# Performance work log

Hardware: AMD Instinct MI355X
Metric: run time of the kernel (lower is better)

Reference implementation:

```python
import jax, jax.numpy as jnp
import numpy as np

B, N, D, H, FF = 4, 1024, 512, 8, 2048
DH = D // H
RPE_HID = 16
COORD_DIM = 2


def _ln(x, g, b, eps=1e-5):
    m = jnp.mean(x, axis=-1, keepdims=True)
    v = jnp.mean((x - m) ** 2, axis=-1, keepdims=True)
    return (x - m) * jax.lax.rsqrt(v + eps) * g + b


def setup_inputs() -> dict:
    key = jax.random.key(0)
    ks = jax.random.split(key, 20)
    s = 0.02
    inp = {
        "x": jax.random.normal(ks[0], (B, N, D), dtype=jnp.float32),
        "coords": jax.random.uniform(ks[1], (B, N, COORD_DIM), dtype=jnp.float32),
        # qkv + output projections
        "Wq": jax.random.normal(ks[2], (D, D), jnp.float32) * s,
        "bq": jnp.zeros((D,), jnp.float32),
        "Wk": jax.random.normal(ks[3], (D, D), jnp.float32) * s,
        "bk": jnp.zeros((D,), jnp.float32),
        "Wv": jax.random.normal(ks[4], (D, D), jnp.float32) * s,
        "bv": jnp.zeros((D,), jnp.float32),
        "Wo": jax.random.normal(ks[5], (D, D), jnp.float32) * s,
        "bo": jnp.zeros((D,), jnp.float32),
        # learned per-head logit scale (Swin-v2 style cosine attention)
        "logit_scale": jnp.full((H, 1, 1), np.log(10.0), jnp.float32),
        # absolute positional embedder PE: Linear(2 -> D)
        "W_pe": jax.random.normal(ks[6], (COORD_DIM, D), jnp.float32) * s,
        "b_pe": jnp.zeros((D,), jnp.float32),
        # relative positional embedder RPE: MLP(2 -> 16 -> H)
        "W_r1": jax.random.normal(ks[7], (COORD_DIM, RPE_HID), jnp.float32) * 0.5,
        "b_r1": jnp.zeros((RPE_HID,), jnp.float32),
        "W_r2": jax.random.normal(ks[8], (RPE_HID, H), jnp.float32) * 0.5,
        "b_r2": jnp.zeros((H,), jnp.float32),
        # layernorm params
        "g_peq": jnp.ones((D,), jnp.float32), "bt_peq": jnp.zeros((D,), jnp.float32),
        "g_pek": jnp.ones((D,), jnp.float32), "bt_pek": jnp.zeros((D,), jnp.float32),
        "g2": jnp.ones((D,), jnp.float32), "bt2": jnp.zeros((D,), jnp.float32),
        "g3": jnp.ones((D,), jnp.float32), "bt3": jnp.zeros((D,), jnp.float32),
        # MLP (bias=False)
        "W_ff1": jax.random.normal(ks[9], (D, FF), jnp.float32) * s,
        "W_ff2": jax.random.normal(ks[10], (FF, D), jnp.float32) * s,
    }
    return inp


def reference(x, coords, Wq, bq, Wk, bk, Wv, bv, Wo, bo, logit_scale,
              W_pe, b_pe, W_r1, b_r1, W_r2, b_r2,
              g_peq, bt_peq, g_pek, bt_pek, g2, bt2, g3, bt3,
              W_ff1, W_ff2):
    # --- PE add + LayerNorm on q and k (self-attention: coords_cross_ = coords)
    pe = coords @ W_pe + b_pe                      # [B,N,D]
    q = _ln(x + pe, g_peq, bt_peq)
    k = _ln(x + pe, g_pek, bt_pek)
    v = x                                          # v is NOT PE-normed in source

    # --- relative-position bias from cartesian coord differences
    rel = coords[:, :, None, :] - coords[:, None, :, :]   # [B,Nq,Nk,2]
    hid = jax.nn.relu(rel @ W_r1 + b_r1)                  # [B,Nq,Nk,16]
    bias = hid @ W_r2 + b_r2                              # [B,Nq,Nk,H]
    bias = jnp.transpose(bias, (0, 3, 1, 2))              # [B,H,Nq,Nk]

    # --- multi-head cosine attention with learned logit scale
    qp = (q @ Wq + bq).reshape(B, N, H, DH)
    kp = (k @ Wk + bk).reshape(B, N, H, DH)
    vp = (v @ Wv + bv).reshape(B, N, H, DH)
    qn = qp / jnp.maximum(jnp.linalg.norm(qp, axis=-1, keepdims=True), 1e-12)
    kn = kp / jnp.maximum(jnp.linalg.norm(kp, axis=-1, keepdims=True), 1e-12)
    scale = jnp.exp(jnp.minimum(logit_scale, jnp.log(100.0)))  # [H,1,1]
    attn = jnp.einsum('bqhd,bkhd->bhqk', qn, kn) * scale[None] + bias
    attn = jax.nn.softmax(attn, axis=-1)
    att_out = jnp.einsum('bhqk,bkhd->bqhd', attn, vp).reshape(B, N, D)
    att_out = att_out @ Wo + bo

    # --- residual + norm + MLP (LeakyReLU 0.2 after each linear) + residual + norm
    x1 = _ln(x + att_out, g2, bt2)
    mlp = jax.nn.leaky_relu(
        jax.nn.leaky_relu(x1 @ W_ff1, 0.2) @ W_ff2, 0.2)
    return _ln(x1 + mlp, g3, bt3)
```

## Files before the change

kernel.cpp:

```cpp
#include <hip/hip_runtime.h>

#define BB 4
#define NN 1024
#define DD 512
#define HH 8
#define DHH 64
#define FFF 2048

typedef __attribute__((ext_vector_type(8))) short bf16x8;
typedef __attribute__((ext_vector_type(4))) float f32x4;

__device__ inline float wave_sum(float v) {
#pragma unroll
  for (int off = 32; off; off >>= 1) v += __shfl_xor(v, off);
  return v;
}

__device__ inline unsigned short cvt_bf16(float f) {
  union { float f; unsigned u; } x;
  x.f = f;
  unsigned r = x.u + 0x7FFFu + ((x.u >> 16) & 1u);
  return (unsigned short)(r >> 16);
}

__device__ __forceinline__ void gl_lds16(const void* g, void* l) {
  __builtin_amdgcn_global_load_lds(
      (__attribute__((address_space(1))) void*)(g),
      (__attribute__((address_space(3))) void*)(l), 16, 0, 0);
}

__global__ __launch_bounds__(256) void wconv_kernel(
    const float* __restrict__ W0, const float* __restrict__ W1,
    const float* __restrict__ W2, const float* __restrict__ W3,
    const float* __restrict__ W4, const float* __restrict__ W5,
    unsigned short* __restrict__ out) {
  int bidx = blockIdx.x;
  const float* W; unsigned short* Wt; int K, N, local;
  if (bidx < 256) {
    int sel = bidx >> 6; local = bidx & 63;
    W = sel == 0 ? W0 : sel == 1 ? W1 : sel == 2 ? W2 : W3;
    K = 512; N = 512; Wt = out + (size_t)sel * 262144;
  } else if (bidx < 512) {
    local = bidx - 256; W = W4; K = 512; N = 2048; Wt = out + 1048576;
  } else {
    local = bidx - 512; W = W5; K = 2048; N = 512; Wt = out + 2097152;
  }
  int ntn = N >> 6;
  int tn = (local & (ntn - 1)) << 6, tk = (local / ntn) << 6;
  __shared__ float tile[64][65];
  int tid = threadIdx.x;
#pragma unroll
  for (int i = 0; i < 16; ++i) {
    int e = tid + i * 256, kk = e >> 6, nn = e & 63;
    tile[kk][nn] = W[(size_t)(tk + kk) * N + tn + nn];
  }
  __syncthreads();
#pragma unroll
  for (int i = 0; i < 16; ++i) {
    int e = tid + i * 256, nn = e >> 6, kk = e & 63;
    Wt[(size_t)(tn + nn) * K + tk + kk] = cvt_bf16(tile[kk][nn]);
  }
}

__global__ __launch_bounds__(256) void bias_kernel(
    const float* __restrict__ coords,
    const float* __restrict__ W_r1, const float* __restrict__ b_r1,
    const float* __restrict__ W_r2, const float* __restrict__ b_r2,
    unsigned short* __restrict__ bias_out) {
  int kt = blockIdx.x, qt = blockIdx.y, b = blockIdx.z;
  int tid = threadIdx.x;
  int q = qt * 64 + (tid >> 2);
  int k0 = kt * 32 + (tid & 3) * 8;
  float cq0 = coords[((size_t)b * NN + q) * 2 + 0];
  float cq1 = coords[((size_t)b * NN + q) * 2 + 1];
  float Aq[16];
#pragma unroll
  for (int l = 0; l < 16; ++l)
    Aq[l] = fmaf(cq0, W_r1[l], fmaf(cq1, W_r1[16 + l], b_r1[l]));
  float ck0[8], ck1[8];
#pragma unroll
  for (int kk = 0; kk < 8; ++kk) {
    ck0[kk] = coords[((size_t)b * NN + k0 + kk) * 2 + 0];
    ck1[kk] = coords[((size_t)b * NN + k0 + kk) * 2 + 1];
  }
  float acc[8][8];
#pragma unroll
  for (int kk = 0; kk < 8; ++kk)
#pragma unroll
    for (int h = 0; h < 8; ++h) acc[kk][h] = b_r2[h];
#pragma unroll
  for (int l = 0; l < 16; ++l) {
    float w1a = W_r1[l], w1b = W_r1[16 + l];
#pragma unroll
    for (int kk = 0; kk < 8; ++kk) {
      float hv = Aq[l] - fmaf(ck0[kk], w1a, ck1[kk] * w1b);
      hv = fmaxf(hv, 0.f);
#pragma unroll
      for (int h = 0; h < 8; ++h)
        acc[kk][h] = fmaf(hv, W_r2[l * HH + h], acc[kk][h]);
    }
  }
#pragma unroll
  for (int h = 0; h < 8; ++h) {
    bf16x8 ov;
#pragma unroll
    for (int kk = 0; kk < 8; ++kk) ov[kk] = (short)cvt_bf16(acc[kk][h]);
    *(bf16x8*)&bias_out[(((size_t)b * HH + h) * NN + q) * NN + k0] = ov;
  }
}

__global__ __launch_bounds__(512) void pe_ln_kernel(
    const float* __restrict__ x, const float* __restrict__ coords,
    const float* __restrict__ W_pe, const float* __restrict__ b_pe,
    const float* __restrict__ g_q, const float* __restrict__ bt_q,
    const float* __restrict__ g_k, const float* __restrict__ bt_k,
    unsigned short* __restrict__ q_lnb, unsigned short* __restrict__ k_lnb,
    unsigned short* __restrict__ x_bf) {
  int row = blockIdx.x;
  int tid = threadIdx.x;
  float c0 = coords[(size_t)row * 2 + 0];
  float c1 = coords[(size_t)row * 2 + 1];
  size_t idx = (size_t)row * DD + tid;
  float xv = x[idx];
  x_bf[idx] = cvt_bf16(xv);
  float val = xv + c0 * W_pe[tid] + c1 * W_pe[DD + tid] + b_pe[tid];

  __shared__ float ws[8], ws2[8];
  float s = wave_sum(val);
  if ((tid & 63) == 0) ws[tid >> 6] = s;
  __syncthreads();
  float mean = 0.f;
#pragma unroll
  for (int w = 0; w < 8; ++w) mean += ws[w];
  mean *= (1.f / DD);
  float dv = val - mean;
  float s2 = wave_sum(dv * dv);
  if ((tid & 63) == 0) ws2[tid >> 6] = s2;
  __syncthreads();
  float var = 0.f;
#pragma unroll
  for (int w = 0; w < 8; ++w) var += ws2[w];
  var *= (1.f / DD);
  float rstd = rsqrtf(var + 1e-5f);
  q_lnb[idx] = cvt_bf16(dv * rstd * g_q[tid] + bt_q[tid]);
  k_lnb[idx] = cvt_bf16(dv * rstd * g_k[tid] + bt_k[tid]);
}

__global__ __launch_bounds__(512) void add_ln_kernel(
    const float* __restrict__ a, const float* __restrict__ r,
    const float* __restrict__ g, const float* __restrict__ bt,
    float* __restrict__ out, unsigned short* __restrict__ out_bf) {
  int row = blockIdx.x;
  int tid = threadIdx.x;
  size_t idx = (size_t)row * DD + tid;
  float val = a[idx] + r[idx];
  __shared__ float ws[8], ws2[8];
  float s = wave_sum(val);
  if ((tid & 63) == 0) ws[tid >> 6] = s;
  __syncthreads();
  float mean = 0.f;
#pragma unroll
  for (int w = 0; w < 8; ++w) mean += ws[w];
  mean *= (1.f / DD);
  float dv = val - mean;
  float s2 = wave_sum(dv * dv);
  if ((tid & 63) == 0) ws2[tid >> 6] = s2;
  __syncthreads();
  float var = 0.f;
#pragma unroll
  for (int w = 0; w < 8; ++w) var += ws2[w];
  var *= (1.f / DD);
  float rstd = rsqrtf(var + 1e-5f);
  float o = dv * rstd * g[tid] + bt[tid];
  out[idx] = o;
  if (out_bf) out_bf[idx] = cvt_bf16(o);
}

template <int ACT, int EPI>
__global__ __launch_bounds__(256) void mgemm_kernel(
    const unsigned short* __restrict__ A, const unsigned short* __restrict__ BT,
    const float* __restrict__ bias, void* __restrict__ C,
    int M, int Nc, int K) {
  __shared__ unsigned short lds[4][8192];
  int tid = threadIdx.x;
  int w = tid >> 6, lane = tid & 63, lg = lane >> 4, lr = lane & 15;
  int bm = blockIdx.y * 128, bn = blockIdx.x * 128;
  int wr = w >> 1, wc = w & 1;

  int segl = lane >> 3;
  int cb = (lane & 7) << 4;

  f32x4 zf = {0.f, 0.f, 0.f, 0.f};
  f32x4 acc[4][4];
#pragma unroll
  for (int mi = 0; mi < 4; ++mi)
#pragma unroll
    for (int ni = 0; ni < 4; ++ni) acc[mi][ni] = zf;

  int nt = K >> 6;

  auto STAGE = [&](int buf, int t) {
    int k0 = t << 6;
#pragma unroll
    for (int i = 0; i < 4; ++i) {
      int seg = w * 4 + i;
      int r = (seg << 3) + segl;
      int csw = cb ^ ((r & 7) << 4);
      const char* ga = (const char*)A + (((size_t)(bm + r) * K + k0) << 1) + csw;
      gl_lds16(ga, &lds[buf * 2][seg << 9]);
      const char* gb = (const char*)BT + (((size_t)(bn + r) * K + k0) << 1) + csw;
      gl_lds16(gb, &lds[buf * 2 + 1][seg << 9]);
    }
  };

  auto COMPUTE = [&](int buf) {
    const unsigned short* As = lds[buf * 2];
    const unsigned short* Bs = lds[buf * 2 + 1];
    bf16x8 af[2][4], bfr[2][4];
#pragma unroll
    for (int kh = 0; kh < 2; ++kh)
#pragma unroll
      for (int mi = 0; mi < 4; ++mi) {
        int r = wr * 64 + mi * 16 + lr;
        int e = (r << 6) + (kh << 5) + (lg << 3);
        af[kh][mi] = *(const bf16x8*)&As[e ^ ((r & 7) << 3)];
        int rb = wc * 64 + mi * 16 + lr;
        int eb = (rb << 6) + (kh << 5) + (lg << 3);
        bfr[kh][mi] = *(const bf16x8*)&Bs[eb ^ ((rb & 7) << 3)];
      }
#pragma unroll
    for (int kh = 0; kh < 2; ++kh)
#pragma unroll
      for (int mi = 0; mi < 4; ++mi)
#pragma unroll
        for (int ni = 0; ni < 4; ++ni)
          acc[mi][ni] = __builtin_amdgcn_mfma_f32_16x16x32_bf16(
              af[kh][mi], bfr[kh][ni], acc[mi][ni], 0, 0, 0);
  };

  STAGE(0, 0);
  __syncthreads();
  for (int t = 0; t < nt; ++t) {
    if (t + 1 < nt) STAGE((t + 1) & 1, t + 1);
    COMPUTE(t & 1);
    __syncthreads();
  }

#pragma unroll
  for (int ni = 0; ni < 4; ++ni) {
    int col = bn + wc * 64 + ni * 16 + lr;
    float bv = bias ? bias[col] : 0.f;
#pragma unroll
    for (int mi = 0; mi < 4; ++mi) {
#pragma unroll
      for (int j = 0; j < 4; ++j) {
        int row = bm + wr * 64 + mi * 16 + lg * 4 + j;
        float v = acc[mi][ni][j] + bv;
        if (ACT == 1) v = v > 0.f ? v : 0.2f * v;
        if (EPI == 1)
          ((unsigned short*)C)[(size_t)row * Nc + col] = cvt_bf16(v);
        else
          ((float*)C)[(size_t)row * Nc + col] = v;
      }
    }
  }
}

__global__ __launch_bounds__(256) void qkv_gemm_kernel(
    const unsigned short* __restrict__ q_lnb,
    const unsigned short* __restrict__ k_lnb,
    const unsigned short* __restrict__ x_bf,
    const unsigned short* __restrict__ wt,
    const float* __restrict__ bq, const float* __restrict__ bk,
    const float* __restrict__ bv_,
    unsigned short* __restrict__ q_bf, unsigned short* __restrict__ k_bf,
    unsigned short* __restrict__ vt_g) {
  int z = blockIdx.z;
  const unsigned short* A = z == 0 ? q_lnb : z == 1 ? k_lnb : x_bf;
  const unsigned short* BT = wt + (size_t)z * 262144;
  const float* bias = z == 0 ? bq : z == 1 ? bk : bv_;

  __shared__ unsigned short lds[4][8192];
  int tid = threadIdx.x;
  int w = tid >> 6, lane = tid & 63, lg = lane >> 4, lr = lane & 15;
  int bm = blockIdx.y * 128, bn = blockIdx.x * 128;
  int wr = w >> 1, wc = w & 1;
  int segl = lane >> 3;
  int cb = (lane & 7) << 4;

  f32x4 zf = {0.f, 0.f, 0.f, 0.f};
  f32x4 acc[4][4];
#pragma unroll
  for (int mi = 0; mi < 4; ++mi)
#pragma unroll
    for (int ni = 0; ni < 4; ++ni) acc[mi][ni] = zf;

  auto STAGE = [&](int buf, int t) {
    int k0 = t << 6;
#pragma unroll
    for (int i = 0; i < 4; ++i) {
      int seg = w * 4 + i;
      int r = (seg << 3) + segl;
      int csw = cb ^ ((r & 7) << 4);
      const char* ga = (const char*)A + (((size_t)(bm + r) * DD + k0) << 1) + csw;
      gl_lds16(ga, &lds[buf * 2][seg << 9]);
      const char* gb = (const char*)BT + (((size_t)(bn + r) * DD + k0) << 1) + csw;
      gl_lds16(gb, &lds[buf * 2 + 1][seg << 9]);
    }
  };
  auto COMPUTE = [&](int buf) {
    const unsigned short* As = lds[buf * 2];
    const unsigned short* Bs = lds[buf * 2 + 1];
    bf16x8 af[2][4], bfr[2][4];
#pragma unroll
    for (int kh = 0; kh < 2; ++kh)
#pragma unroll
      for (int mi = 0; mi < 4; ++mi) {
        int r = wr * 64 + mi * 16 + lr;
        int e = (r << 6) + (kh << 5) + (lg << 3);
        af[kh][mi] = *(const bf16x8*)&As[e ^ ((r & 7) << 3)];
        int rb = wc * 64 + mi * 16 + lr;
        int eb = (rb << 6) + (kh << 5) + (lg << 3);
        bfr[kh][mi] = *(const bf16x8*)&Bs[eb ^ ((rb & 7) << 3)];
      }
#pragma unroll
    for (int kh = 0; kh < 2; ++kh)
#pragma unroll
      for (int mi = 0; mi < 4; ++mi)
#pragma unroll
        for (int ni = 0; ni < 4; ++ni)
          acc[mi][ni] = __builtin_amdgcn_mfma_f32_16x16x32_bf16(
              af[kh][mi], bfr[kh][ni], acc[mi][ni], 0, 0, 0);
  };

  STAGE(0, 0);
  __syncthreads();
  for (int t = 0; t < 8; ++t) {
    if (t + 1 < 8) STAGE((t + 1) & 1, t + 1);
    COMPUTE(t & 1);
    __syncthreads();
  }

  int h = (bn >> 6) + wc;
  float bvf[4];
#pragma unroll
  for (int ni = 0; ni < 4; ++ni) bvf[ni] = bias[bn + wc * 64 + ni * 16 + lr];
#pragma unroll
  for (int mi = 0; mi < 4; ++mi) {
#pragma unroll
    for (int j = 0; j < 4; ++j) {
      float vals[4]; float ss = 0.f;
#pragma unroll
      for (int ni = 0; ni < 4; ++ni) {
        float v = acc[mi][ni][j] + bvf[ni];
        vals[ni] = v;
        ss = fmaf(v, v, ss);
      }
      int row = bm + wr * 64 + mi * 16 + lg * 4 + j;
      int b_ = row >> 10, n_ = row & (NN - 1);
      if (z <= 1) {
        ss += __shfl_xor(ss, 1);
        ss += __shfl_xor(ss, 2);
        ss += __shfl_xor(ss, 4);
        ss += __shfl_xor(ss, 8);
        float rn = 1.f / fmaxf(sqrtf(ss), 1e-12f);
        unsigned short* ob = (z == 0 ? q_bf : k_bf) +
                             (((size_t)b_ * HH + h) * NN + n_) * DHH;
#pragma unroll
        for (int ni = 0; ni < 4; ++ni)
          ob[ni * 16 + lr] = cvt_bf16(vals[ni] * rn);
      } else {
#pragma unroll
        for (int ni = 0; ni < 4; ++ni)
          vt_g[(((size_t)b_ * HH + h) * DHH + ni * 16 + lr) * NN + n_] =
              cvt_bf16(vals[ni]);
      }
    }
  }
}

template <int NSPLIT>
__global__ __launch_bounds__(256) void attn_wave_kernel(
    const unsigned short* __restrict__ qb, const unsigned short* __restrict__ kb,
    const unsigned short* __restrict__ vtg,
    const unsigned short* __restrict__ bias_g,
    const float* __restrict__ logit_scale,
    unsigned short* __restrict__ attb,
    unsigned short* __restrict__ part, int nb) {
  int qt = blockIdx.x, h = blockIdx.y;
  int b = blockIdx.z % nb, sp = blockIdx.z / nb;
  int tid = threadIdx.x;
  int w = tid >> 6, lane = tid & 63;
  int lg = lane >> 4, lr = lane & 15;

  __shared__ unsigned short pl[4][1024];

  const size_t bh = ((size_t)b * HH + h) * NN;
  const size_t vbase = ((size_t)b * HH + h) * DHH * NN;
  const int NT = (NN / 64) / NSPLIT;
  const int kt0 = sp * NT;

  int q_glob = qt * 64 + w * 16 + lr;
  bf16x8 aq0 = *(const bf16x8*)&qb[(bh + q_glob) * DHH + lg * 8];
  bf16x8 aq1 = *(const bf16x8*)&qb[(bh + q_glob) * DHH + 32 + lg * 8];

  float scale_h = __expf(fminf(logit_scale[h], 4.605170185988091f));

  const unsigned short* brow[4];
#pragma unroll
  for (int r = 0; r < 4; ++r)
    brow[r] = &bias_g[(bh + qt * 64 + w * 16 + lg * 4 + r) * NN + lr];

  float m_run[4] = {-1e30f, -1e30f, -1e30f, -1e30f};
  float l_run[4] = {0.f, 0.f, 0.f, 0.f};
  f32x4 zf = {0.f, 0.f, 0.f, 0.f};
  f32x4 acc_o[4] = {zf, zf, zf, zf};

  unsigned short bu[4][4];
#pragma unroll
  for (int r = 0; r < 4; ++r)
#pragma unroll
    for (int kc = 0; kc < 4; ++kc) bu[kc][r] = brow[r][kt0 * 64 + kc * 16];

#pragma unroll 2
  for (int t = 0; t < NT; ++t) {
    int ktg = kt0 + t;

    f32x4 s_acc[4];
#pragma unroll
    for (int kc = 0; kc < 4; ++kc) {
      const unsigned short* krow =
          &kb[(bh + ktg * 64 + kc * 16 + lr) * DHH + lg * 8];
      bf16x8 bk0 = *(const bf16x8*)krow;
      bf16x8 bk1 = *(const bf16x8*)(krow + 32);
      s_acc[kc] = __builtin_amdgcn_mfma_f32_16x16x32_bf16(aq0, bk0, zf, 0, 0, 0);
      s_acc[kc] = __builtin_amdgcn_mfma_f32_16x16x32_bf16(aq1, bk1, s_acc[kc], 0, 0, 0);
    }

    unsigned short bu2[4][4];
    if (t + 1 < NT) {
#pragma unroll
      for (int r = 0; r < 4; ++r)
#pragma unroll
        for (int kc = 0; kc < 4; ++kc)
          bu2[kc][r] = brow[r][(ktg + 1) * 64 + kc * 16];
    }

#pragma unroll
    for (int kc = 0; kc < 4; ++kc)
#pragma unroll
      for (int r = 0; r < 4; ++r) {
        float bf_ = __uint_as_float(((unsigned)bu[kc][r]) << 16);
        s_acc[kc][r] = fmaf(s_acc[kc][r], scale_h, bf_);
      }

    float pf[4][4];
#pragma unroll
    for (int r = 0; r < 4; ++r) {
      float mx = fmaxf(fmaxf(s_acc[0][r], s_acc[1][r]),
                       fmaxf(s_acc[2][r], s_acc[3][r]));
      mx = fmaxf(mx, __shfl_xor(mx, 1));
      mx = fmaxf(mx, __shfl_xor(mx, 2));
      mx = fmaxf(mx, __shfl_xor(mx, 4));
      mx = fmaxf(mx, __shfl_xor(mx, 8));
      float m_new = fmaxf(m_run[r], mx);
      float alpha = __expf(m_run[r] - m_new);
      m_run[r] = m_new;
      float ps = 0.f;
#pragma unroll
      for (int kc = 0; kc < 4; ++kc) {
        float p = __expf(s_acc[kc][r] - m_new);
        pf[kc][r] = p;
        ps += p;
      }
      l_run[r] = l_run[r] * alpha + ps;
#pragma unroll
      for (int ds = 0; ds < 4; ++ds) acc_o[ds][r] *= alpha;
    }

#pragma unroll
    for (int kc = 0; kc < 4; ++kc)
#pragma unroll
      for (int r = 0; r < 4; ++r) {
        int q = lg * 4 + r;
        pl[w][(q * 64 + kc * 16 + lr) ^ ((q & 7) << 3)] = cvt_bf16(pf[kc][r]);
      }

#pragma unroll
    for (int ka = 0; ka < 2; ++ka) {
      bf16x8 pa = *(const bf16x8*)&pl[w][(lr * 64 + ka * 32 + lg * 8) ^
                                         ((lr & 7) << 3)];
#pragma unroll
      for (int ds = 0; ds < 4; ++ds) {
        int d = ds * 16 + lr;
        bf16x8 bv = *(const bf16x8*)&vtg[vbase + (size_t)d * NN +
                                         ktg * 64 + ka * 32 + lg * 8];
        acc_o[ds] = __builtin_amdgcn_mfma_f32_16x16x32_bf16(pa, bv, acc_o[ds], 0, 0, 0);
      }
    }

    if (t + 1 < NT) {
#pragma unroll
      for (int r = 0; r < 4; ++r)
#pragma unroll
        for (int kc = 0; kc < 4; ++kc) bu[kc][r] = bu2[kc][r];
    }
  }

#pragma unroll
  for (int r = 0; r < 4; ++r) {
    l_run[r] += __shfl_xor(l_run[r], 1);
    l_run[r] += __shfl_xor(l_run[r], 2);
    l_run[r] += __shfl_xor(l_run[r], 4);
    l_run[r] += __shfl_xor(l_run[r], 8);
  }

  if (NSPLIT == 1) {
#pragma unroll
    for (int ds = 0; ds < 4; ++ds)
#pragma unroll
      for (int r = 0; r < 4; ++r) {
        int qg = qt * 64 + w * 16 + lg * 4 + r;
        attb[((size_t)b * NN + qg) * DD + h * DHH + ds * 16 + lr] =
            cvt_bf16(acc_o[ds][r] / l_run[r]);
      }
  } else {
#pragma unroll
    for (int r = 0; r < 4; ++r) {
      int qg = qt * 64 + w * 16 + lg * 4 + r;
      size_t idx = ((size_t)(sp * nb + b) * HH + h) * NN + qg;
      unsigned short* pr = part + idx * 68;
#pragma unroll
      for (int ds = 0; ds < 4; ++ds)
        pr[ds * 16 + lr] = cvt_bf16(acc_o[ds][r]);
      if (lr == 0) {
        *(float*)(pr + 64) = m_run[r];
        *(float*)(pr + 66) = l_run[r];
      }
    }
  }
}

__global__ __launch_bounds__(256) void combine_kernel(
    const unsigned short* __restrict__ part, unsigned short* __restrict__ attb,
    int nb) {
  int tid = threadIdx.x;
  int w = tid >> 6, d = tid & 63;
  int row = blockIdx.x * 4 + w;
  int b = row >> 13, rem = row & 8191, h = rem >> 10, n = rem & (NN - 1);
  size_t i0 = ((size_t)b * HH + h) * NN + n;
  size_t i1 = i0 + (size_t)nb * HH * NN;
  const unsigned short* p0 = part + i0 * 68;
  const unsigned short* p1 = part + i1 * 68;
  float m0 = *(const float*)(p0 + 64), l0 = *(const float*)(p0 + 66);
  float m1 = *(const float*)(p1 + 64), l1 = *(const float*)(p1 + 66);
  float ms = fmaxf(m0, m1);
  float w0 = __expf(m0 - ms), w1 = __expf(m1 - ms);
  float a0 = __uint_as_float(((unsigned)p0[d]) << 16);
  float a1 = __uint_as_float(((unsigned)p1[d]) << 16);
  float o = (a0 * w0 + a1 * w1) / (l0 * w0 + l1 * w1);
  attb[((size_t)b * NN + n) * DD + h * DHH + d] = cvt_bf16(o);
}

extern "C" void kernel_launch(void* const* d_in, const int* in_sizes, int n_in,
                              void* d_out, int out_size, void* d_ws, size_t ws_size,
                              hipStream_t stream) {
  const float* x      = (const float*)d_in[0];
  const float* coords = (const float*)d_in[1];
  const float* Wq = (const float*)d_in[2];  const float* bq = (const float*)d_in[3];
  const float* Wk = (const float*)d_in[4];  const float* bk = (const float*)d_in[5];
  const float* Wv = (const float*)d_in[6];  const float* bv = (const float*)d_in[7];
  const float* Wo = (const float*)d_in[8];  const float* bo = (const float*)d_in[9];
  const float* logit_scale = (const float*)d_in[10];
  const float* W_pe = (const float*)d_in[11]; const float* b_pe = (const float*)d_in[12];
  const float* W_r1 = (const float*)d_in[13]; const float* b_r1 = (const float*)d_in[14];
  const float* W_r2 = (const float*)d_in[15]; const float* b_r2 = (const float*)d_in[16];
  const float* g_peq = (const float*)d_in[17]; const float* bt_peq = (const float*)d_in[18];
  const float* g_pek = (const float*)d_in[19]; const float* bt_pek = (const float*)d_in[20];
  const float* g2 = (const float*)d_in[21]; const float* bt2 = (const float*)d_in[22];
  const float* g3 = (const float*)d_in[23]; const float* bt3 = (const float*)d_in[24];
  const float* W_ff1 = (const float*)d_in[25];
  const float* W_ff2 = (const float*)d_in[26];
  float* out = (float*)d_out;

  const size_t T = (size_t)BB * NN;
  char* wsb = (char*)d_ws;
  const size_t U = 4u * 1024u * 1024u;

  unsigned short* wt_all = (unsigned short*)(wsb + 0 * U);
  unsigned short* WoT   = wt_all + 786432;
  unsigned short* Wff1T = wt_all + 1048576;
  unsigned short* Wff2T = wt_all + 2097152;
  unsigned short* q_lnb = (unsigned short*)(wsb + 2 * U);
  unsigned short* k_lnb = (unsigned short*)(wsb + 3 * U);
  unsigned short* x_bf  = (unsigned short*)(wsb + 4 * U);
  unsigned short* q_bf  = (unsigned short*)(wsb + 5 * U);
  unsigned short* k_bf  = (unsigned short*)(wsb + 6 * U);
  unsigned short* v_bf  = (unsigned short*)(wsb + 7 * U);
  unsigned short* att_bf = (unsigned short*)(wsb + 8 * U);
  float* proj = (float*)(wsb + 9 * U);
  float* x1   = (float*)(wsb + 11 * U);
  unsigned short* x1_bf = (unsigned short*)(wsb + 13 * U);
  unsigned short* hid_bf = (unsigned short*)(wsb + 2 * U);
  float* mlp  = (float*)(wsb + 9 * U);
  unsigned short* part_ws = (unsigned short*)(wsb + 2 * U);
  unsigned short* bias_ws = (unsigned short*)(wsb + 9 * U);

  const int full_path = (ws_size >= 25 * U) ? 1 : 0;

  wconv_kernel<<<dim3(768), dim3(256), 0, stream>>>(
      Wq, Wk, Wv, Wo, W_ff1, W_ff2, wt_all);

  pe_ln_kernel<<<dim3(T), dim3(512), 0, stream>>>(
      x, coords, W_pe, b_pe, g_peq, bt_peq, g_pek, bt_pek, q_lnb, k_lnb, x_bf);

  qkv_gemm_kernel<<<dim3(DD / 128, T / 128, 3), dim3(256), 0, stream>>>(
      q_lnb, k_lnb, x_bf, wt_all, bq, bk, bv, q_bf, k_bf, v_bf);

  if (full_path) {
    bias_kernel<<<dim3(NN / 32, NN / 64, BB), dim3(256), 0, stream>>>(
        coords, W_r1, b_r1, W_r2, b_r2, bias_ws);
    attn_wave_kernel<2><<<dim3(NN / 64, HH, 2 * BB), dim3(256), 0, stream>>>(
        q_bf, k_bf, v_bf, bias_ws, logit_scale, nullptr, part_ws, BB);
    combine_kernel<<<dim3(BB * HH * NN / 4), dim3(256), 0, stream>>>(
        part_ws, att_bf, BB);
  } else {
    for (int b = 0; b < BB; ++b) {
      bias_kernel<<<dim3(NN / 32, NN / 64, 1), dim3(256), 0, stream>>>(
          coords + (size_t)b * NN * 2, W_r1, b_r1, W_r2, b_r2, bias_ws);
      attn_wave_kernel<1><<<dim3(NN / 64, HH, 1), dim3(256), 0, stream>>>(
          q_bf + (size_t)b * HH * NN * DHH, k_bf + (size_t)b * HH * NN * DHH,
          v_bf + (size_t)b * HH * DHH * NN, bias_ws, logit_scale,
          att_bf + (size_t)b * NN * DD, nullptr, 1);
    }
  }

  mgemm_kernel<0, 0><<<dim3(DD / 128, T / 128), dim3(256), 0, stream>>>(
      att_bf, WoT, bo, proj, (int)T, DD, DD);

  add_ln_kernel<<<dim3(T), dim3(512), 0, stream>>>(x, proj, g2, bt2, x1, x1_bf);

  mgemm_kernel<1, 1><<<dim3(FFF / 128, T / 128), dim3(256), 0, stream>>>(
      x1_bf, Wff1T, nullptr, hid_bf, (int)T, FFF, DD);
  mgemm_kernel<1, 0><<<dim3(DD / 128, T / 128), dim3(256), 0, stream>>>(
      hid_bf, Wff2T, nullptr, mlp, (int)T, DD, FFF);

  add_ln_kernel<<<dim3(T), dim3(512), 0, stream>>>(x1, mlp, g3, bt3, out, nullptr);
}
```

Measured before the change: 198.1 us.

## Store RPE bias in 64x64 tiles and stage it through LDS

The bias kernel now writes the relative-position bias in contiguous 64x64 tiles per (batch, head, q-tile, k-tile) instead of row-major [Nq,Nk]. The attention kernel loads each tile with coalesced 16-byte vector loads and writes it into a double-buffered, XOR-swizzled per-wave LDS buffer, then reads scalar values from LDS. The goal is to replace the 16 strided 2-byte global loads per lane per tile with wide coalesced loads. In exchange it uses more LDS and drops the unroll-by-2 pragma.

```diff
diff --git a/kernel.cpp b/kernel.cpp
--- a/kernel.cpp
+++ b/kernel.cpp
@@ -69,7 +69,8 @@
     unsigned short* __restrict__ bias_out) {
   int kt = blockIdx.x, qt = blockIdx.y, b = blockIdx.z;
   int tid = threadIdx.x;
-  int q = qt * 64 + (tid >> 2);
+  int qL = tid >> 2;
+  int q = qt * 64 + qL;
   int k0 = kt * 32 + (tid & 3) * 8;
   float cq0 = coords[((size_t)b * NN + q) * 2 + 0];
   float cq1 = coords[((size_t)b * NN + q) * 2 + 1];
@@ -100,12 +101,14 @@
         acc[kk][h] = fmaf(hv, W_r2[l * HH + h], acc[kk][h]);
     }
   }
+  int elem = qL * 64 + (kt & 1) * 32 + (tid & 3) * 8;
 #pragma unroll
   for (int h = 0; h < 8; ++h) {
     bf16x8 ov;
 #pragma unroll
     for (int kk = 0; kk < 8; ++kk) ov[kk] = (short)cvt_bf16(acc[kk][h]);
-    *(bf16x8*)&bias_out[(((size_t)b * HH + h) * NN + q) * NN + k0] = ov;
+    size_t tile = (((size_t)b * HH + h) * 16 + qt) * 16 + (kt >> 1);
+    *(bf16x8*)&bias_out[tile * 4096 + elem] = ov;
   }
 }
 
@@ -383,7 +386,7 @@
 __global__ __launch_bounds__(256) void attn_wave_kernel(
     const unsigned short* __restrict__ qb, const unsigned short* __restrict__ kb,
     const unsigned short* __restrict__ vtg,
-    const unsigned short* __restrict__ bias_g,
+    const unsigned short* __restrict__ bias_t,
     const float* __restrict__ logit_scale,
     unsigned short* __restrict__ attb,
     unsigned short* __restrict__ part, int nb) {
@@ -393,38 +396,49 @@
   int w = tid >> 6, lane = tid & 63;
   int lg = lane >> 4, lr = lane & 15;
 
+  __shared__ unsigned short bl[4][2][1024];
   __shared__ unsigned short pl[4][1024];
 
   const size_t bh = ((size_t)b * HH + h) * NN;
   const size_t vbase = ((size_t)b * HH + h) * DHH * NN;
   const int NT = (NN / 64) / NSPLIT;
   const int kt0 = sp * NT;
+  const unsigned short* bsrc0 =
+      bias_t + ((((size_t)b * HH + h) * 16 + qt) * 16 + kt0) * 4096 +
+      w * 1024 + lane * 8;
+
+  int rr0 = lane >> 3, rr1 = 8 + (lane >> 3);
+  int d0 = (rr0 * 8 + ((lane & 7) ^ (rr0 & 7))) * 8;
+  int d1 = (rr1 * 8 + ((lane & 7) ^ (rr1 & 7))) * 8;
 
   int q_glob = qt * 64 + w * 16 + lr;
   bf16x8 aq0 = *(const bf16x8*)&qb[(bh + q_glob) * DHH + lg * 8];
   bf16x8 aq1 = *(const bf16x8*)&qb[(bh + q_glob) * DHH + 32 + lg * 8];
 
   float scale_h = __expf(fminf(logit_scale[h], 4.605170185988091f));
-
-  const unsigned short* brow[4];
-#pragma unroll
-  for (int r = 0; r < 4; ++r)
-    brow[r] = &bias_g[(bh + qt * 64 + w * 16 + lg * 4 + r) * NN + lr];
 
   float m_run[4] = {-1e30f, -1e30f, -1e30f, -1e30f};
   float l_run[4] = {0.f, 0.f, 0.f, 0.f};
   f32x4 zf = {0.f, 0.f, 0.f, 0.f};
   f32x4 acc_o[4] = {zf, zf, zf, zf};
 
-  unsigned short bu[4][4];
-#pragma unroll
-  for (int r = 0; r < 4; ++r)
-#pragma unroll
-    for (int kc = 0; kc < 4; ++kc) bu[kc][r] = brow[r][kt0 * 64 + kc * 16];
-
-#pragma unroll 2
+  {
+    bf16x8 br0 = *(const bf16x8*)bsrc0;
+    bf16x8 br1 = *(const bf16x8*)(bsrc0 + 512);
+    *(bf16x8*)&bl[w][0][d0] = br0;
+    *(bf16x8*)&bl[w][0][d1] = br1;
+  }
+
   for (int t = 0; t < NT; ++t) {
+    int cur = t & 1;
     int ktg = kt0 + t;
+
+    bf16x8 nb0, nb1;
+    if (t + 1 < NT) {
+      const unsigned short* bs = bsrc0 + (size_t)(t + 1) * 4096;
+      nb0 = *(const bf16x8*)bs;
+      nb1 = *(const bf16x8*)(bs + 512);
+    }
 
     f32x4 s_acc[4];
 #pragma unroll
@@ -437,20 +451,14 @@
       s_acc[kc] = __builtin_amdgcn_mfma_f32_16x16x32_bf16(aq1, bk1, s_acc[kc], 0, 0, 0);
     }
 
-    unsigned short bu2[4][4];
-    if (t + 1 < NT) {
-#pragma unroll
-      for (int r = 0; r < 4; ++r)
-#pragma unroll
-        for (int kc = 0; kc < 4; ++kc)
-          bu2[kc][r] = brow[r][(ktg + 1) * 64 + kc * 16];
-    }
-
 #pragma unroll
     for (int kc = 0; kc < 4; ++kc)
 #pragma unroll
       for (int r = 0; r < 4; ++r) {
-        float bf_ = __uint_as_float(((unsigned)bu[kc][r]) << 16);
+        int rr = lg * 4 + r;
+        unsigned short ub =
+            bl[w][cur][(rr * 64 + kc * 16 + lr) ^ ((rr & 7) << 3)];
+        float bf_ = __uint_as_float(((unsigned)ub) << 16);
         s_acc[kc][r] = fmaf(s_acc[kc][r], scale_h, bf_);
       }
 
@@ -500,10 +508,8 @@
     }
 
     if (t + 1 < NT) {
-#pragma unroll
-      for (int r = 0; r < 4; ++r)
-#pragma unroll
-        for (int kc = 0; kc < 4; ++kc) bu[kc][r] = bu2[kc][r];
+      *(bf16x8*)&bl[w][cur ^ 1][d0] = nb0;
+      *(bf16x8*)&bl[w][cur ^ 1][d1] = nb1;
     }
   }
 
```

After: 195.4 us. About the same (-1.4%).

## Fuse relative-position bias MLP into attention kernel instead of materializing bias

Applied to the files above, without the earlier changes.

Removes the separate bias kernel, which wrote a bf16 [B,H,N,N] bias tensor that attention then read back. The per-position first-layer terms (Aq with bias, Ck) are now precomputed in the LN kernel, and attention recomputes the 16-hidden ReLU MLP inline per score for its own head. This cuts a large HBM write and read at the cost of roughly 16 extra FMA/max ops per score per head, which repeats the hidden-layer work across the 8 heads. The workspace-size fallback path is dropped and the split-2 path always runs.

```diff
diff --git a/kernel.cpp b/kernel.cpp
--- a/kernel.cpp
+++ b/kernel.cpp
@@ -62,64 +62,25 @@
   }
 }
 
-__global__ __launch_bounds__(256) void bias_kernel(
-    const float* __restrict__ coords,
-    const float* __restrict__ W_r1, const float* __restrict__ b_r1,
-    const float* __restrict__ W_r2, const float* __restrict__ b_r2,
-    unsigned short* __restrict__ bias_out) {
-  int kt = blockIdx.x, qt = blockIdx.y, b = blockIdx.z;
-  int tid = threadIdx.x;
-  int q = qt * 64 + (tid >> 2);
-  int k0 = kt * 32 + (tid & 3) * 8;
-  float cq0 = coords[((size_t)b * NN + q) * 2 + 0];
-  float cq1 = coords[((size_t)b * NN + q) * 2 + 1];
-  float Aq[16];
-#pragma unroll
-  for (int l = 0; l < 16; ++l)
-    Aq[l] = fmaf(cq0, W_r1[l], fmaf(cq1, W_r1[16 + l], b_r1[l]));
-  float ck0[8], ck1[8];
-#pragma unroll
-  for (int kk = 0; kk < 8; ++kk) {
-    ck0[kk] = coords[((size_t)b * NN + k0 + kk) * 2 + 0];
-    ck1[kk] = coords[((size_t)b * NN + k0 + kk) * 2 + 1];
-  }
-  float acc[8][8];
-#pragma unroll
-  for (int kk = 0; kk < 8; ++kk)
-#pragma unroll
-    for (int h = 0; h < 8; ++h) acc[kk][h] = b_r2[h];
-#pragma unroll
-  for (int l = 0; l < 16; ++l) {
-    float w1a = W_r1[l], w1b = W_r1[16 + l];
-#pragma unroll
-    for (int kk = 0; kk < 8; ++kk) {
-      float hv = Aq[l] - fmaf(ck0[kk], w1a, ck1[kk] * w1b);
-      hv = fmaxf(hv, 0.f);
-#pragma unroll
-      for (int h = 0; h < 8; ++h)
-        acc[kk][h] = fmaf(hv, W_r2[l * HH + h], acc[kk][h]);
-    }
-  }
-#pragma unroll
-  for (int h = 0; h < 8; ++h) {
-    bf16x8 ov;
-#pragma unroll
-    for (int kk = 0; kk < 8; ++kk) ov[kk] = (short)cvt_bf16(acc[kk][h]);
-    *(bf16x8*)&bias_out[(((size_t)b * HH + h) * NN + q) * NN + k0] = ov;
-  }
-}
-
 __global__ __launch_bounds__(512) void pe_ln_kernel(
     const float* __restrict__ x, const float* __restrict__ coords,
     const float* __restrict__ W_pe, const float* __restrict__ b_pe,
+    const float* __restrict__ W_r1, const float* __restrict__ b_r1,
     const float* __restrict__ g_q, const float* __restrict__ bt_q,
     const float* __restrict__ g_k, const float* __restrict__ bt_k,
     unsigned short* __restrict__ q_lnb, unsigned short* __restrict__ k_lnb,
-    unsigned short* __restrict__ x_bf) {
+    unsigned short* __restrict__ x_bf,
+    float* __restrict__ AqT, float* __restrict__ CkT) {
   int row = blockIdx.x;
   int tid = threadIdx.x;
   float c0 = coords[(size_t)row * 2 + 0];
   float c1 = coords[(size_t)row * 2 + 1];
+  if (tid < 32) {
+    int l = tid & 15;
+    float ck = fmaf(c0, W_r1[l], c1 * W_r1[16 + l]);
+    if (tid < 16) AqT[(size_t)row * 16 + l] = ck + b_r1[l];
+    else          CkT[(size_t)row * 16 + l] = ck;
+  }
   size_t idx = (size_t)row * DD + tid;
   float xv = x[idx];
   x_bf[idx] = cvt_bf16(xv);
@@ -383,7 +344,8 @@
 __global__ __launch_bounds__(256) void attn_wave_kernel(
     const unsigned short* __restrict__ qb, const unsigned short* __restrict__ kb,
     const unsigned short* __restrict__ vtg,
-    const unsigned short* __restrict__ bias_g,
+    const float* __restrict__ AqT, const float* __restrict__ CkT,
+    const float* __restrict__ W_r2, const float* __restrict__ b_r2,
     const float* __restrict__ logit_scale,
     unsigned short* __restrict__ attb,
     unsigned short* __restrict__ part, int nb) {
@@ -405,26 +367,34 @@
   bf16x8 aq1 = *(const bf16x8*)&qb[(bh + q_glob) * DHH + 32 + lg * 8];
 
   float scale_h = __expf(fminf(logit_scale[h], 4.605170185988091f));
-
-  const unsigned short* brow[4];
-#pragma unroll
-  for (int r = 0; r < 4; ++r)
-    brow[r] = &bias_g[(bh + qt * 64 + w * 16 + lg * 4 + r) * NN + lr];
+  float br2h = b_r2[h];
+  float w2h[16];
+#pragma unroll
+  for (int l = 0; l < 16; ++l) w2h[l] = W_r2[l * HH + h];
+
+  float Aq[4][16];
+#pragma unroll
+  for (int r = 0; r < 4; ++r) {
+    const float* ap =
+        &AqT[((size_t)b * NN + qt * 64 + w * 16 + lg * 4 + r) * 16];
+#pragma unroll
+    for (int l4 = 0; l4 < 4; ++l4)
+      *(f32x4*)&Aq[r][l4 * 4] = *(const f32x4*)&ap[l4 * 4];
+  }
 
   float m_run[4] = {-1e30f, -1e30f, -1e30f, -1e30f};
   float l_run[4] = {0.f, 0.f, 0.f, 0.f};
   f32x4 zf = {0.f, 0.f, 0.f, 0.f};
   f32x4 acc_o[4] = {zf, zf, zf, zf};
 
-  unsigned short bu[4][4];
-#pragma unroll
-  for (int r = 0; r < 4; ++r)
-#pragma unroll
-    for (int kc = 0; kc < 4; ++kc) bu[kc][r] = brow[r][kt0 * 64 + kc * 16];
-
-#pragma unroll 2
   for (int t = 0; t < NT; ++t) {
     int ktg = kt0 + t;
+    const float* ckbase = &CkT[((size_t)b * NN + ktg * 64 + lr) * 16];
+    f32x4 ckA[4], ckB[4];
+#pragma unroll
+    for (int i = 0; i < 4; ++i) ckA[i] = *(const f32x4*)&ckbase[i * 4];
+#pragma unroll
+    for (int i = 0; i < 4; ++i) ckB[i] = *(const f32x4*)&ckbase[256 + i * 4];
 
     f32x4 s_acc[4];
 #pragma unroll
@@ -437,22 +407,27 @@
       s_acc[kc] = __builtin_amdgcn_mfma_f32_16x16x32_bf16(aq1, bk1, s_acc[kc], 0, 0, 0);
     }
 
-    unsigned short bu2[4][4];
-    if (t + 1 < NT) {
-#pragma unroll
-      for (int r = 0; r < 4; ++r)
-#pragma unroll
-        for (int kc = 0; kc < 4; ++kc)
-          bu2[kc][r] = brow[r][(ktg + 1) * 64 + kc * 16];
-    }
-
-#pragma unroll
-    for (int kc = 0; kc < 4; ++kc)
+    auto BIAS = [&](int kc, const f32x4* ck) {
 #pragma unroll
       for (int r = 0; r < 4; ++r) {
-        float bf_ = __uint_as_float(((unsigned)bu[kc][r]) << 16);
-        s_acc[kc][r] = fmaf(s_acc[kc][r], scale_h, bf_);
-      }
+        float bias = br2h;
+#pragma unroll
+        for (int l = 0; l < 16; ++l) {
+          float hv = Aq[r][l] - ck[l >> 2][l & 3];
+          hv = fmaxf(hv, 0.f);
+          bias = fmaf(hv, w2h[l], bias);
+        }
+        s_acc[kc][r] = fmaf(s_acc[kc][r], scale_h, bias);
+      }
+    };
+    BIAS(0, ckA);
+#pragma unroll
+    for (int i = 0; i < 4; ++i) ckA[i] = *(const f32x4*)&ckbase[512 + i * 4];
+    BIAS(1, ckB);
+#pragma unroll
+    for (int i = 0; i < 4; ++i) ckB[i] = *(const f32x4*)&ckbase[768 + i * 4];
+    BIAS(2, ckA);
+    BIAS(3, ckB);
 
     float pf[4][4];
 #pragma unroll
@@ -497,13 +472,6 @@
                                          ktg * 64 + ka * 32 + lg * 8];
         acc_o[ds] = __builtin_amdgcn_mfma_f32_16x16x32_bf16(pa, bv, acc_o[ds], 0, 0, 0);
       }
-    }
-
-    if (t + 1 < NT) {
-#pragma unroll
-      for (int r = 0; r < 4; ++r)
-#pragma unroll
-        for (int kc = 0; kc < 4; ++kc) bu[kc][r] = bu2[kc][r];
     }
   }
 
@@ -604,36 +572,24 @@
   unsigned short* hid_bf = (unsigned short*)(wsb + 2 * U);
   float* mlp  = (float*)(wsb + 9 * U);
   unsigned short* part_ws = (unsigned short*)(wsb + 2 * U);
-  unsigned short* bias_ws = (unsigned short*)(wsb + 9 * U);
-
-  const int full_path = (ws_size >= 25 * U) ? 1 : 0;
+  float* AqT = (float*)(wsb + 13 * U);
+  float* CkT = (float*)(wsb + 13 * U + 262144);
 
   wconv_kernel<<<dim3(768), dim3(256), 0, stream>>>(
       Wq, Wk, Wv, Wo, W_ff1, W_ff2, wt_all);
 
   pe_ln_kernel<<<dim3(T), dim3(512), 0, stream>>>(
-      x, coords, W_pe, b_pe, g_peq, bt_peq, g_pek, bt_pek, q_lnb, k_lnb, x_bf);
+      x, coords, W_pe, b_pe, W_r1, b_r1, g_peq, bt_peq, g_pek, bt_pek,
+      q_lnb, k_lnb, x_bf, AqT, CkT);
 
   qkv_gemm_kernel<<<dim3(DD / 128, T / 128, 3), dim3(256), 0, stream>>>(
       q_lnb, k_lnb, x_bf, wt_all, bq, bk, bv, q_bf, k_bf, v_bf);
 
-  if (full_path) {
-    bias_kernel<<<dim3(NN / 32, NN / 64, BB), dim3(256), 0, stream>>>(
-        coords, W_r1, b_r1, W_r2, b_r2, bias_ws);
-    attn_wave_kernel<2><<<dim3(NN / 64, HH, 2 * BB), dim3(256), 0, stream>>>(
-        q_bf, k_bf, v_bf, bias_ws, logit_scale, nullptr, part_ws, BB);
-    combine_kernel<<<dim3(BB * HH * NN / 4), dim3(256), 0, stream>>>(
-        part_ws, att_bf, BB);
-  } else {
-    for (int b = 0; b < BB; ++b) {
-      bias_kernel<<<dim3(NN / 32, NN / 64, 1), dim3(256), 0, stream>>>(
-          coords + (size_t)b * NN * 2, W_r1, b_r1, W_r2, b_r2, bias_ws);
-      attn_wave_kernel<1><<<dim3(NN / 64, HH, 1), dim3(256), 0, stream>>>(
-          q_bf + (size_t)b * HH * NN * DHH, k_bf + (size_t)b * HH * NN * DHH,
-          v_bf + (size_t)b * HH * DHH * NN, bias_ws, logit_scale,
-          att_bf + (size_t)b * NN * DD, nullptr, 1);
-    }
-  }
+  attn_wave_kernel<2><<<dim3(NN / 64, HH, 2 * BB), dim3(256), 0, stream>>>(
+      q_bf, k_bf, v_bf, AqT, CkT, W_r2, b_r2, logit_scale,
+      nullptr, part_ws, BB);
+  combine_kernel<<<dim3(BB * HH * NN / 4), dim3(256), 0, stream>>>(
+      part_ws, att_bf, BB);
 
   mgemm_kernel<0, 0><<<dim3(DD / 128, T / 128), dim3(256), 0, stream>>>(
       att_bf, WoT, bo, proj, (int)T, DD, DD);
```

Result: slower. 221.7 us (+11.9%).

## Store V row-major and transpose tiles through LDS inside attention kernel

Applied to the files above, without the earlier changes.

The QKV GEMM now writes V in the same [B,H,N,DH] row-major layout as Q and K instead of a strided transposed scatter, which should make the V store coalesced. The attention kernel then loads each 64x64 V tile cooperatively, transposes it into a swizzled LDS buffer, and reads the MFMA B operand from LDS rather than from global memory. This costs two block-wide barriers per key tile, extra LDS traffic, and scalar LDS writes during the transpose. The loop unroll pragma is dropped and the bias prefetch is moved later in the loop body.

```diff
diff --git a/kernel.cpp b/kernel.cpp
--- a/kernel.cpp
+++ b/kernel.cpp
@@ -274,7 +274,7 @@
     const float* __restrict__ bq, const float* __restrict__ bk,
     const float* __restrict__ bv_,
     unsigned short* __restrict__ q_bf, unsigned short* __restrict__ k_bf,
-    unsigned short* __restrict__ vt_g) {
+    unsigned short* __restrict__ v_bf) {
   int z = blockIdx.z;
   const unsigned short* A = z == 0 ? q_lnb : z == 1 ? k_lnb : x_bf;
   const unsigned short* BT = wt + (size_t)z * 262144;
@@ -356,33 +356,29 @@
         vals[ni] = v;
         ss = fmaf(v, v, ss);
       }
-      int row = bm + wr * 64 + mi * 16 + lg * 4 + j;
-      int b_ = row >> 10, n_ = row & (NN - 1);
+      float rn = 1.f;
       if (z <= 1) {
         ss += __shfl_xor(ss, 1);
         ss += __shfl_xor(ss, 2);
         ss += __shfl_xor(ss, 4);
         ss += __shfl_xor(ss, 8);
-        float rn = 1.f / fmaxf(sqrtf(ss), 1e-12f);
-        unsigned short* ob = (z == 0 ? q_bf : k_bf) +
-                             (((size_t)b_ * HH + h) * NN + n_) * DHH;
-#pragma unroll
-        for (int ni = 0; ni < 4; ++ni)
-          ob[ni * 16 + lr] = cvt_bf16(vals[ni] * rn);
-      } else {
-#pragma unroll
-        for (int ni = 0; ni < 4; ++ni)
-          vt_g[(((size_t)b_ * HH + h) * DHH + ni * 16 + lr) * NN + n_] =
-              cvt_bf16(vals[ni]);
-      }
+        rn = 1.f / fmaxf(sqrtf(ss), 1e-12f);
+      }
+      int row = bm + wr * 64 + mi * 16 + lg * 4 + j;
+      int b_ = row >> 10, n_ = row & (NN - 1);
+      unsigned short* ob = (z == 0 ? q_bf : z == 1 ? k_bf : v_bf) +
+                           (((size_t)b_ * HH + h) * NN + n_) * DHH;
+#pragma unroll
+      for (int ni = 0; ni < 4; ++ni)
+        ob[ni * 16 + lr] = cvt_bf16(vals[ni] * rn);
     }
   }
 }
 
 template <int NSPLIT>
-__global__ __launch_bounds__(256) void attn_wave_kernel(
+__global__ __launch_bounds__(256) void attn_kernel(
     const unsigned short* __restrict__ qb, const unsigned short* __restrict__ kb,
-    const unsigned short* __restrict__ vtg,
+    const unsigned short* __restrict__ vb,
     const unsigned short* __restrict__ bias_g,
     const float* __restrict__ logit_scale,
     unsigned short* __restrict__ attb,
@@ -393,10 +389,10 @@
   int w = tid >> 6, lane = tid & 63;
   int lg = lane >> 4, lr = lane & 15;
 
+  __shared__ unsigned short vt[64 * 64];
   __shared__ unsigned short pl[4][1024];
 
   const size_t bh = ((size_t)b * HH + h) * NN;
-  const size_t vbase = ((size_t)b * HH + h) * DHH * NN;
   const int NT = (NN / 64) / NSPLIT;
   const int kt0 = sp * NT;
 
@@ -404,12 +400,13 @@
   bf16x8 aq0 = *(const bf16x8*)&qb[(bh + q_glob) * DHH + lg * 8];
   bf16x8 aq1 = *(const bf16x8*)&qb[(bh + q_glob) * DHH + 32 + lg * 8];
 
+  const unsigned short* brow[4];
+#pragma unroll
+  for (int r = 0; r < 4; ++r) {
+    int qg = qt * 64 + w * 16 + lg * 4 + r;
+    brow[r] = &bias_g[(bh + qg) * NN + lr];
+  }
   float scale_h = __expf(fminf(logit_scale[h], 4.605170185988091f));
-
-  const unsigned short* brow[4];
-#pragma unroll
-  for (int r = 0; r < 4; ++r)
-    brow[r] = &bias_g[(bh + qt * 64 + w * 16 + lg * 4 + r) * NN + lr];
 
   float m_run[4] = {-1e30f, -1e30f, -1e30f, -1e30f};
   float l_run[4] = {0.f, 0.f, 0.f, 0.f};
@@ -422,9 +419,22 @@
 #pragma unroll
     for (int kc = 0; kc < 4; ++kc) bu[kc][r] = brow[r][kt0 * 64 + kc * 16];
 
-#pragma unroll 2
   for (int t = 0; t < NT; ++t) {
     int ktg = kt0 + t;
+
+    __syncthreads();
+#pragma unroll
+    for (int it = 0; it < 2; ++it) {
+      int kl = it * 32 + (tid & 31);
+      int d0 = (tid >> 5) * 8;
+      bf16x8 vv = *(const bf16x8*)&vb[(bh + ktg * 64 + kl) * DHH + d0];
+#pragma unroll
+      for (int j = 0; j < 8; ++j) {
+        int d = d0 + j;
+        vt[(d * 64 + kl) ^ ((d & 7) << 3)] = (unsigned short)vv[j];
+      }
+    }
+    __syncthreads();
 
     f32x4 s_acc[4];
 #pragma unroll
@@ -437,15 +447,6 @@
       s_acc[kc] = __builtin_amdgcn_mfma_f32_16x16x32_bf16(aq1, bk1, s_acc[kc], 0, 0, 0);
     }
 
-    unsigned short bu2[4][4];
-    if (t + 1 < NT) {
-#pragma unroll
-      for (int r = 0; r < 4; ++r)
-#pragma unroll
-        for (int kc = 0; kc < 4; ++kc)
-          bu2[kc][r] = brow[r][(ktg + 1) * 64 + kc * 16];
-    }
-
 #pragma unroll
     for (int kc = 0; kc < 4; ++kc)
 #pragma unroll
@@ -453,6 +454,15 @@
         float bf_ = __uint_as_float(((unsigned)bu[kc][r]) << 16);
         s_acc[kc][r] = fmaf(s_acc[kc][r], scale_h, bf_);
       }
+
+    unsigned short bu2[4][4];
+    if (t + 1 < NT) {
+#pragma unroll
+      for (int r = 0; r < 4; ++r)
+#pragma unroll
+        for (int kc = 0; kc < 4; ++kc)
+          bu2[kc][r] = brow[r][(ktg + 1) * 64 + kc * 16];
+    }
 
     float pf[4][4];
 #pragma unroll
@@ -493,8 +503,7 @@
 #pragma unroll
       for (int ds = 0; ds < 4; ++ds) {
         int d = ds * 16 + lr;
-        bf16x8 bv = *(const bf16x8*)&vtg[vbase + (size_t)d * NN +
-                                         ktg * 64 + ka * 32 + lg * 8];
+        bf16x8 bv = *(const bf16x8*)&vt[(d * 64 + ka * 32 + lg * 8) ^ ((d & 7) << 3)];
         acc_o[ds] = __builtin_amdgcn_mfma_f32_16x16x32_bf16(pa, bv, acc_o[ds], 0, 0, 0);
       }
     }
@@ -620,7 +629,7 @@
   if (full_path) {
     bias_kernel<<<dim3(NN / 32, NN / 64, BB), dim3(256), 0, stream>>>(
         coords, W_r1, b_r1, W_r2, b_r2, bias_ws);
-    attn_wave_kernel<2><<<dim3(NN / 64, HH, 2 * BB), dim3(256), 0, stream>>>(
+    attn_kernel<2><<<dim3(NN / 64, HH, 2 * BB), dim3(256), 0, stream>>>(
         q_bf, k_bf, v_bf, bias_ws, logit_scale, nullptr, part_ws, BB);
     combine_kernel<<<dim3(BB * HH * NN / 4), dim3(256), 0, stream>>>(
         part_ws, att_bf, BB);
@@ -628,9 +637,9 @@
     for (int b = 0; b < BB; ++b) {
       bias_kernel<<<dim3(NN / 32, NN / 64, 1), dim3(256), 0, stream>>>(
           coords + (size_t)b * NN * 2, W_r1, b_r1, W_r2, b_r2, bias_ws);
-      attn_wave_kernel<1><<<dim3(NN / 64, HH, 1), dim3(256), 0, stream>>>(
+      attn_kernel<1><<<dim3(NN / 64, HH, 1), dim3(256), 0, stream>>>(
           q_bf + (size_t)b * HH * NN * DHH, k_bf + (size_t)b * HH * NN * DHH,
-          v_bf + (size_t)b * HH * DHH * NN, bias_ws, logit_scale,
+          v_bf + (size_t)b * HH * NN * DHH, bias_ws, logit_scale,
           att_bf + (size_t)b * NN * DD, nullptr, 1);
     }
   }
```

New measurement: 190.2 us. 4.0% less time.
